# Optimization experiments

Hardware: AMD Instinct MI355X
Metric: run time of the kernel (lower is better)

## Reference

```python
import jax, jax.numpy as jnp
import numpy as np

N, E, IN, H, C, ED = 50000, 800000, 128, 4, 64, 4
NEG_SLOPE = 0.2


def setup_inputs() -> dict:
    key = jax.random.key(0)
    ks = iter(jax.random.split(key, 40))
    def p(shape, s=0.05):
        return jax.random.normal(next(ks), shape, jnp.float32) * s
    inp = dict(
        x=jax.random.normal(next(ks), (N, IN), jnp.float32),
        edge_index=jax.random.randint(next(ks), (2, E), 0, N),
        edge_attr=jax.random.normal(next(ks), (E, ED), jnp.float32),
        # GATConv layer 1 (concat=True)
        W1=p((IN, H * C)), att_src1=p((H, C)), att_dst1=p((H, C)),
        We1=p((ED, H * C)), att_e1=p((H, C)), b1=p((H * C,)),
        g1=jnp.ones((H * C,), jnp.float32), be1=jnp.zeros((H * C,), jnp.float32),
        # GATConv layer 2 (concat=False -> mean over heads)
        W2=p((H * C, H * C)), att_src2=p((H, C)), att_dst2=p((H, C)),
        We2=p((ED, H * C)), att_e2=p((H, C)), b2=p((C,)),
        g2=jnp.ones((C,), jnp.float32), be2=jnp.zeros((C,), jnp.float32),
        # skip / MLP head
        skip_W=p((IN, C)), skip_b=p((C,)),
        fc1_W=p((C, C // 2)), fc1_b=p((C // 2,)),
        fc2_W=p((C // 2, 1)), fc2_b=p((1,)),
    )
    return inp


def _add_self_loops(edge_index, edge_attr, n):
    # PyG GATConv default: add_self_loops=True, fill_value='mean'
    src, dst = edge_index[0], edge_index[1]
    sums = jax.ops.segment_sum(edge_attr, dst, num_segments=n)
    cnt = jax.ops.segment_sum(jnp.ones((edge_attr.shape[0], 1), edge_attr.dtype), dst, num_segments=n)
    mean_attr = sums / jnp.maximum(cnt, 1.0)
    loop = jnp.arange(n)
    src = jnp.concatenate([src, loop])
    dst = jnp.concatenate([dst, loop])
    ea = jnp.concatenate([edge_attr, mean_attr], axis=0)
    return src, dst, ea


def _gat_layer(x, src, dst, ea, W, a_src, a_dst, We, a_e, bias, n, concat):
    xs = (x @ W).reshape(n, H, C)                     # [N,H,C]
    alpha_src = (xs * a_src).sum(-1)                  # [N,H]
    alpha_dst = (xs * a_dst).sum(-1)                  # [N,H]
    ep = (ea @ We).reshape(-1, H, C)                  # [Et,H,C]
    alpha_e = (ep * a_e).sum(-1)                      # [Et,H]
    alpha = jax.nn.leaky_relu(alpha_src[src] + alpha_dst[dst] + alpha_e, NEG_SLOPE)
    # segment softmax over destination nodes
    m = jax.ops.segment_max(alpha, dst, num_segments=n)
    alpha = jnp.exp(alpha - m[dst])
    denom = jax.ops.segment_sum(alpha, dst, num_segments=n)
    alpha = alpha / (denom[dst] + 1e-16)
    out = jax.ops.segment_sum(xs[src] * alpha[:, :, None], dst, num_segments=n)  # [N,H,C]
    out = out.reshape(n, H * C) if concat else out.mean(axis=1)
    return out + bias


def _bn(x, g, b):
    mu = x.mean(0)
    var = x.var(0)
    return (x - mu) * jax.lax.rsqrt(var + 1e-5) * g + b


def reference(x, edge_index, edge_attr, W1, att_src1, att_dst1, We1, att_e1, b1, g1, be1,
              W2, att_src2, att_dst2, We2, att_e2, b2, g2, be2,
              skip_W, skip_b, fc1_W, fc1_b, fc2_W, fc2_b):
    n = x.shape[0]
    src, dst, ea = _add_self_loops(edge_index, edge_attr, n)
    residual = x @ skip_W + skip_b
    h = _gat_layer(x, src, dst, ea, W1, att_src1, att_dst1, We1, att_e1, b1, n, True)
    h = jax.nn.elu(_bn(h, g1, be1))
    h = _gat_layer(h, src, dst, ea, W2, att_src2, att_dst2, We2, att_e2, b2, n, False)
    h = jax.nn.elu(_bn(h, g2, be2))
    h = h + residual
    h = jax.nn.relu(h @ fc1_W + fc1_b)
    h = jax.nn.softplus(h @ fc2_W + fc2_b)
    return h.squeeze(-1)
```

## Files before the change

kernel.cpp:

```cpp
#include <hip/hip_runtime.h>
#include <math.h>

static constexpr int N_NODES = 50000;
static constexpr int N_EDGES = 800000;
static constexpr int IN_F = 128;
static constexpr int CH = 64;
static constexpr int HC = 256;
static constexpr float NEG_SLOPE = 0.2f;

typedef __attribute__((ext_vector_type(8))) short bf16x8;
typedef __attribute__((ext_vector_type(4))) float f32x4;

__device__ __forceinline__ unsigned pack_bf(float a, float b) {
    unsigned ua = __float_as_uint(a) + 0x8000u;
    unsigned ub = __float_as_uint(b) + 0x8000u;
    return __builtin_amdgcn_perm(ub, ua, 0x07060302u);
}
__device__ __forceinline__ float bflo(unsigned u) { return __uint_as_float(u << 16); }
__device__ __forceinline__ float bfhi(unsigned u) { return __uint_as_float(u & 0xffff0000u); }
__device__ __forceinline__ float bfs(unsigned short u) {
    return __uint_as_float((unsigned)u << 16);
}
__device__ __forceinline__ float elu(float v) { return v > 0.f ? v : __expf(v) - 1.0f; }

__device__ __forceinline__ int sigma(int p) { return ((p & 15) << 4) | (p >> 4); }

static constexpr int EB_BLK = (N_EDGES + 255) / 256;
static constexpr int CONV_ITEMS = 106496 + 32;
static constexpr int CONV_BLK = (CONV_ITEMS + 255) / 256;
static constexpr int GEMM_BLKS = (N_NODES + 63) / 64;

__global__ void hist_conv(const int* __restrict__ ei, int* __restrict__ deg,
                          const float* __restrict__ W1, const float* __restrict__ W2,
                          const float* __restrict__ Ws, const float* __restrict__ We1,
                          const float* __restrict__ atte1, const float* __restrict__ We2,
                          const float* __restrict__ atte2, unsigned short* __restrict__ WT1,
                          unsigned short* __restrict__ WT2, unsigned short* __restrict__ WTs,
                          float* __restrict__ weff) {
    if (blockIdx.x < EB_BLK) {
        int e = blockIdx.x * 256 + threadIdx.x;
        if (e < N_EDGES) atomicAdd(&deg[ei[N_EDGES + e]], 1);
        return;
    }
    int t = (blockIdx.x - EB_BLK) * 256 + threadIdx.x;
    if (t < 32768) {
        int k = t >> 8, n = t & 255;
        unsigned u = __float_as_uint(W1[t]) + 0x8000u;
        WT1[n * 128 + k] = (unsigned short)(u >> 16);
    } else if (t < 98304) {
        int u2 = t - 32768;
        int k = u2 >> 8, n = u2 & 255;
        unsigned u = __float_as_uint(W2[u2]) + 0x8000u;
        WT2[n * 256 + sigma(k)] = (unsigned short)(u >> 16);
    } else if (t < 106496) {
        int u2 = t - 98304;
        int k = u2 >> 6, n = u2 & 63;
        unsigned u = __float_as_uint(Ws[u2]) + 0x8000u;
        WTs[n * 128 + k] = (unsigned short)(u >> 16);
    } else if (t < 106496 + 32) {
        int idx = t - 106496;
        const float* We = idx < 16 ? We1 : We2;
        const float* ae = idx < 16 ? atte1 : atte2;
        int j = idx & 15;
        int d = j >> 2, h = j & 3;
        float s = 0.f;
        for (int c = 0; c < CH; ++c) s += We[d * HC + h * CH + c] * ae[h * CH + c];
        weff[idx] = s;
    }
}

__global__ void scan_block(const int* __restrict__ deg, int* __restrict__ rowptr,
                           int* __restrict__ bsum) {
    __shared__ int s[256];
    int tid = threadIdx.x;
    int i = blockIdx.x * 256 + tid;
    int v = (i < N_NODES) ? deg[i] : 0;
    s[tid] = v;
    __syncthreads();
    for (int off = 1; off < 256; off <<= 1) {
        int t = (tid >= off) ? s[tid - off] : 0;
        __syncthreads();
        s[tid] += t;
        __syncthreads();
    }
    if (i < N_NODES) rowptr[i] = s[tid] - v;
    if (tid == 255) bsum[blockIdx.x] = s[255];
}

__global__ void scan_add2(int* __restrict__ rowptr, const int* __restrict__ bsum,
                          int* __restrict__ fillc, int nb) {
    __shared__ int s[256];
    int tid = threadIdx.x;
    int v = (tid < nb) ? bsum[tid] : 0;
    s[tid] = v;
    __syncthreads();
    for (int off = 1; off < 256; off <<= 1) {
        int t = (tid >= off) ? s[tid - off] : 0;
        __syncthreads();
        s[tid] += t;
        __syncthreads();
    }
    int boff = (blockIdx.x == 0) ? 0 : s[blockIdx.x - 1];
    int i = blockIdx.x * 256 + tid;
    if (i < N_NODES) {
        rowptr[i] += boff;
        fillc[i] = 0;
    }
    if (i == N_NODES) rowptr[N_NODES] = N_EDGES;
}

template <int K, bool ABF, bool BN, bool SKIP, bool FILL>
__global__ __launch_bounds__(256) void gemm_mfma_att(
    const void* __restrict__ Av, const unsigned short* __restrict__ BT,
    const float* __restrict__ colsum, const float* __restrict__ g,
    const float* __restrict__ be, float invM,
    const unsigned short* __restrict__ BTs, const float* __restrict__ skip_b,
    float* __restrict__ residual,
    const float* __restrict__ att_src, const float* __restrict__ att_dst,
    unsigned short* __restrict__ xsb, float* __restrict__ asrc, float* __restrict__ adst,
    int M, const int* __restrict__ ei, const float4* __restrict__ ea,
    const int* __restrict__ rowptr, int* __restrict__ fillc, int* __restrict__ csr_src,
    int* __restrict__ csr_dst, float4* __restrict__ eaperm) {
    if constexpr (FILL) {
        if (blockIdx.x >= GEMM_BLKS) {
            int e = (blockIdx.x - GEMM_BLKS) * 256 + threadIdx.x;
            if (e < N_EDGES) {
                int s = ei[e];
                int t = ei[N_EDGES + e];
                int p = atomicAdd(&fillc[t], 1);
                int i = rowptr[t] + p;
                csr_src[i] = s;
                csr_dst[i] = t;
                eaperm[i] = ea[e];
            }
            return;
        }
    }
    constexpr int NT = 16;
    __shared__ float s_scale[256], s_shift[256];
    if constexpr (BN) {
        int c = threadIdx.x;
        int tc = sigma(c);
        float mean = colsum[c] * invM;
        float var = colsum[256 + c] * invM - mean * mean;
        float sc = g[tc] * rsqrtf(var + 1e-5f);
        s_scale[c] = sc;
        s_shift[c] = be[tc] - mean * sc;
        __syncthreads();
    }
    const int lane = threadIdx.x & 63;
    const int wid = threadIdx.x >> 6;
    const int r0 = blockIdx.x * 64 + wid * 16;
    const int lr = lane & 15;
    const int kg = lane >> 4;
    f32x4 acc[NT] = {};
    f32x4 accS[4] = {};
    const float* af = (const float*)Av;
    const unsigned short* ab = (const unsigned short*)Av;
    int rr = r0 + lr;
    if (rr >= M) rr = M - 1;
    const size_t rowoff = (size_t)rr * K + kg * 8;
    const unsigned short* brow = BT + (size_t)lr * K + kg * 8;
    const unsigned short* brow_s = SKIP ? BTs + (size_t)lr * K + kg * 8 : nullptr;
    for (int k0 = 0; k0 < K; k0 += 32) {
        float4 sc0, sc1, sh0, sh1;
        if constexpr (BN) {
            sc0 = *reinterpret_cast<const float4*>(&s_scale[k0 + kg * 8]);
            sc1 = *reinterpret_cast<const float4*>(&s_scale[k0 + kg * 8 + 4]);
            sh0 = *reinterpret_cast<const float4*>(&s_shift[k0 + kg * 8]);
            sh1 = *reinterpret_cast<const float4*>(&s_shift[k0 + kg * 8 + 4]);
        }
        bf16x8 a;
        if constexpr (!ABF) {
            const float4 lo = *reinterpret_cast<const float4*>(af + rowoff + k0);
            const float4 hi = *reinterpret_cast<const float4*>(af + rowoff + k0 + 4);
            union { bf16x8 v; unsigned u[4]; } fa;
            fa.u[0] = pack_bf(lo.x, lo.y);
            fa.u[1] = pack_bf(lo.z, lo.w);
            fa.u[2] = pack_bf(hi.x, hi.y);
            fa.u[3] = pack_bf(hi.z, hi.w);
            a = fa.v;
        } else {
            union { bf16x8 v; unsigned short us[8]; unsigned u[4]; } fa;
            fa.v = *reinterpret_cast<const bf16x8*>(ab + rowoff + k0);
            if constexpr (BN) {
                float f0 = elu(fmaf(bfs(fa.us[0]), sc0.x, sh0.x));
                float f1 = elu(fmaf(bfs(fa.us[1]), sc0.y, sh0.y));
                float f2 = elu(fmaf(bfs(fa.us[2]), sc0.z, sh0.z));
                float f3 = elu(fmaf(bfs(fa.us[3]), sc0.w, sh0.w));
                float f4 = elu(fmaf(bfs(fa.us[4]), sc1.x, sh1.x));
                float f5 = elu(fmaf(bfs(fa.us[5]), sc1.y, sh1.y));
                float f6 = elu(fmaf(bfs(fa.us[6]), sc1.z, sh1.z));
                float f7 = elu(fmaf(bfs(fa.us[7]), sc1.w, sh1.w));
                fa.u[0] = pack_bf(f0, f1);
                fa.u[1] = pack_bf(f2, f3);
                fa.u[2] = pack_bf(f4, f5);
                fa.u[3] = pack_bf(f6, f7);
            }
            a = fa.v;
        }
#pragma unroll
        for (int c = 0; c < NT; ++c) {
            bf16x8 b = *reinterpret_cast<const bf16x8*>(brow + (size_t)c * 16 * K + k0);
            acc[c] = __builtin_amdgcn_mfma_f32_16x16x32_bf16(a, b, acc[c], 0, 0, 0);
        }
        if constexpr (SKIP) {
#pragma unroll
            for (int c = 0; c < 4; ++c) {
                bf16x8 b = *reinterpret_cast<const bf16x8*>(brow_s + (size_t)c * 16 * K + k0);
                accS[c] = __builtin_amdgcn_mfma_f32_16x16x32_bf16(a, b, accS[c], 0, 0, 0);
            }
        }
    }
    float attS[NT], attD[NT];
#pragma unroll
    for (int c = 0; c < NT; ++c) {
        attS[c] = att_src[c * 16 + lr];
        attD[c] = att_dst[c * 16 + lr];
    }
#pragma unroll
    for (int j = 0; j < 4; ++j) {
        int row = r0 + kg * 4 + j;
        bool valid = row < M;
        uint4 ua, ub;
        ua.x = pack_bf(acc[0][j], acc[1][j]);
        ua.y = pack_bf(acc[2][j], acc[3][j]);
        ua.z = pack_bf(acc[4][j], acc[5][j]);
        ua.w = pack_bf(acc[6][j], acc[7][j]);
        ub.x = pack_bf(acc[8][j], acc[9][j]);
        ub.y = pack_bf(acc[10][j], acc[11][j]);
        ub.z = pack_bf(acc[12][j], acc[13][j]);
        ub.w = pack_bf(acc[14][j], acc[15][j]);
        if (valid) {
            uint4* dst = reinterpret_cast<uint4*>(xsb + (size_t)row * HC) + lr * 2;
            dst[0] = ua;
            dst[1] = ub;
        }
        if constexpr (SKIP) {
            if (valid) {
#pragma unroll
                for (int c = 0; c < 4; ++c) {
                    int col = c * 16 + lr;
                    residual[(size_t)row * CH + col] = accS[c][j] + skip_b[col];
                }
            }
        }
#pragma unroll
        for (int h = 0; h < 4; ++h) {
            float ps = acc[4 * h + 0][j] * attS[4 * h + 0] +
                       acc[4 * h + 1][j] * attS[4 * h + 1] +
                       acc[4 * h + 2][j] * attS[4 * h + 2] +
                       acc[4 * h + 3][j] * attS[4 * h + 3];
            float pd = acc[4 * h + 0][j] * attD[4 * h + 0] +
                       acc[4 * h + 1][j] * attD[4 * h + 1] +
                       acc[4 * h + 2][j] * attD[4 * h + 2] +
                       acc[4 * h + 3][j] * attD[4 * h + 3];
#pragma unroll
            for (int mk = 1; mk < 16; mk <<= 1) {
                ps += __shfl_xor(ps, mk);
                pd += __shfl_xor(pd, mk);
            }
            if (valid && lr == 0) {
                asrc[row * 4 + h] = ps;
                adst[row * 4 + h] = pd;
            }
        }
    }
}

__global__ __launch_bounds__(256) void edge_w(
    const int* __restrict__ csr_src, const int* __restrict__ csr_dst,
    const float4* __restrict__ eaperm, const float* __restrict__ weff,
    const float4* __restrict__ asrcv, const float4* __restrict__ adstv,
    uint4* __restrict__ pw) {
    int i = blockIdx.x * 256 + threadIdx.x;
    if (i >= N_EDGES) return;
    int s = csr_src[i];
    int t = csr_dst[i];
    const float4 v = eaperm[i];
    const float4 as4 = asrcv[s];
    const float4 ad4 = adstv[t];
    const float asl[4] = {as4.x, as4.y, as4.z, as4.w};
    const float adl[4] = {ad4.x, ad4.y, ad4.z, ad4.w};
    float p[4], aev[4];
#pragma unroll
    for (int h = 0; h < 4; ++h) {
        float ae = v.x * weff[h] + v.y * weff[4 + h] + v.z * weff[8 + h] + v.w * weff[12 + h];
        float l = asl[h] + adl[h] + ae;
        l = fmaxf(l, NEG_SLOPE * l);
        p[h] = __expf(l);
        aev[h] = ae;
    }
    pw[i] = make_uint4(pack_bf(p[0], p[1]), pack_bf(p[2], p[3]),
                       pack_bf(aev[0], aev[1]), pack_bf(aev[2], aev[3]));
}

template <bool MEAN>
__global__ __launch_bounds__(256) void gat_node(
    const int* __restrict__ rowptr, const int* __restrict__ csr_src,
    const uint4* __restrict__ pw, const float4* __restrict__ asrcv,
    const float4* __restrict__ adstv, const uint2* __restrict__ xsb,
    float* __restrict__ zbuf, void* __restrict__ outp) {
    if (blockIdx.x == 0) {
        zbuf[threadIdx.x] = 0.f;
        zbuf[256 + threadIdx.x] = 0.f;
    }
    int t = blockIdx.x * 4 + (threadIdx.x >> 6);
    if (t >= N_NODES) return;
    const int lane = threadIdx.x & 63;
    const int h = lane & 3;
    const unsigned sh = (h & 1) ? 0u : 16u;
    const bool hiW = (h & 2) != 0;
    const int start = rowptr[t], end = rowptr[t + 1];
    const int deg = end - start;
    const uint2* xl = xsb + lane;
    float acc0 = 0.f, acc1 = 0.f, acc2 = 0.f, acc3 = 0.f;
    float psum = 0.f, aesum = 0.f;
    int i = start;
    for (; i + 8 <= end; i += 8) {
        uint2 f[8];
        float p[8], ae[8];
#pragma unroll
        for (int j = 0; j < 8; ++j) {
            int s = csr_src[i + j];
            f[j] = xl[(size_t)s * 64];
            const uint4 w = pw[i + j];
            unsigned pword = hiW ? w.y : w.x;
            unsigned aeword = hiW ? w.w : w.z;
            p[j] = __uint_as_float((pword << sh) & 0xffff0000u);
            ae[j] = __uint_as_float((aeword << sh) & 0xffff0000u);
        }
#pragma unroll
        for (int j = 0; j < 8; ++j) {
            psum += p[j];
            aesum += ae[j];
            acc0 += bflo(f[j].x) * p[j];
            acc1 += bfhi(f[j].x) * p[j];
            acc2 += bflo(f[j].y) * p[j];
            acc3 += bfhi(f[j].y) * p[j];
        }
    }
    for (; i < end; ++i) {
        int s = csr_src[i];
        uint2 f = xl[(size_t)s * 64];
        const uint4 w = pw[i];
        unsigned pword = hiW ? w.y : w.x;
        unsigned aeword = hiW ? w.w : w.z;
        float p = __uint_as_float((pword << sh) & 0xffff0000u);
        float ae = __uint_as_float((aeword << sh) & 0xffff0000u);
        psum += p;
        aesum += ae;
        acc0 += bflo(f.x) * p;
        acc1 += bfhi(f.x) * p;
        acc2 += bflo(f.y) * p;
        acc3 += bfhi(f.y) * p;
    }
    const float inv_deg = deg > 0 ? 1.0f / (float)deg : 1.0f;
    const float4 as4 = asrcv[t];
    const float4 ad4 = adstv[t];
    float asl = h == 0 ? as4.x : h == 1 ? as4.y : h == 2 ? as4.z : as4.w;
    float adl = h == 0 ? ad4.x : h == 1 ? ad4.y : h == 2 ? ad4.z : ad4.w;
    float l = asl + adl + aesum * inv_deg;
    l = fmaxf(l, NEG_SLOPE * l);
    const float pself = __expf(l);
    uint2 sf = xl[(size_t)t * 64];
    acc0 += bflo(sf.x) * pself;
    acc1 += bfhi(sf.x) * pself;
    acc2 += bflo(sf.y) * pself;
    acc3 += bfhi(sf.y) * pself;
    const float inv = 1.0f / (psum + pself + 1e-16f);
    acc0 *= inv; acc1 *= inv; acc2 *= inv; acc3 *= inv;
    if constexpr (MEAN) {
        acc0 += __shfl_xor(acc0, 1); acc0 += __shfl_xor(acc0, 2);
        acc1 += __shfl_xor(acc1, 1); acc1 += __shfl_xor(acc1, 2);
        acc2 += __shfl_xor(acc2, 1); acc2 += __shfl_xor(acc2, 2);
        acc3 += __shfl_xor(acc3, 1); acc3 += __shfl_xor(acc3, 2);
        if (h == 0) {
            int q = lane >> 2;
            float* o = reinterpret_cast<float*>(outp) + (size_t)t * CH + q;
            o[0] = 0.25f * acc0;
            o[16] = 0.25f * acc1;
            o[32] = 0.25f * acc2;
            o[48] = 0.25f * acc3;
        }
    } else {
        reinterpret_cast<uint2*>(outp)[(size_t)t * 64 + lane] =
            make_uint2(pack_bf(acc0, acc1), pack_bf(acc2, acc3));
    }
}

__global__ void colstats_bf(const unsigned short* __restrict__ X, float* __restrict__ sum,
                            float* __restrict__ sumsq, int M) {
    int c = threadIdx.x;
    int r0 = blockIdx.x * 256;
    int r1 = min(M, r0 + 256);
    float s = 0.f, q = 0.f;
    for (int r = r0; r < r1; ++r) {
        float v = bfs(X[(size_t)r * HC + c]);
        s += v;
        q += v * v;
    }
    atomicAdd(&sum[c], s);
    atomicAdd(&sumsq[c], q);
}

template <int F>
__global__ void colstats(const float* __restrict__ X, float* __restrict__ sum,
                         float* __restrict__ sumsq, int M) {
    const int NG = 256 / F;
    int c = threadIdx.x % F;
    int g = threadIdx.x / F;
    int r0 = blockIdx.x * 256;
    int r1 = min(M, r0 + 256);
    float s = 0.f, q = 0.f;
    for (int r = r0 + g; r < r1; r += NG) {
        float v = X[(size_t)r * F + c];
        s += v;
        q += v * v;
    }
    atomicAdd(&sum[c], s);
    atomicAdd(&sumsq[c], q);
}

__global__ __launch_bounds__(256) void head_mlp(
    const float* __restrict__ h2, const float* __restrict__ colsum,
    const float* __restrict__ g2, const float* __restrict__ be2, float invM,
    const float* __restrict__ residual, const float* __restrict__ fc1W,
    const float* __restrict__ fc1b, const float* __restrict__ fc2W,
    const float* __restrict__ fc2b, float* __restrict__ out) {
    __shared__ float s_sc[CH], s_sh[CH];
    if (threadIdx.x < CH) {
        int c = threadIdx.x;
        float mean = colsum[c] * invM;
        float var = colsum[256 + c] * invM - mean * mean;
        float sc = g2[c] * rsqrtf(var + 1e-5f);
        s_sc[c] = sc;
        s_sh[c] = be2[c] - mean * sc;
    }
    __syncthreads();
    int n = blockIdx.x * 4 + (threadIdx.x >> 6);
    if (n >= N_NODES) return;
    int w = threadIdx.x >> 6;
    int lane = threadIdx.x & 63;
    __shared__ float hrow[4][64];
    float v = fmaf(h2[(size_t)n * CH + lane], s_sc[lane], s_sh[lane]);
    v = elu(v) + residual[(size_t)n * CH + lane];
    hrow[w][lane] = v;
    float p = 0.f;
    if (lane < 32) {
        float acc = fc1b[lane];
#pragma unroll
        for (int k = 0; k < CH; ++k) acc = fmaf(hrow[w][k], fc1W[k * 32 + lane], acc);
        acc = fmaxf(acc, 0.f);
        p = acc * fc2W[lane];
    }
    for (int off = 16; off > 0; off >>= 1) p += __shfl_down(p, off);
    if (lane == 0) {
        float z = p + fc2b[0];
        out[n] = z > 20.f ? z : log1pf(expf(z));
    }
}

extern "C" void kernel_launch(void* const* d_in, const int* in_sizes, int n_in, void* d_out,
                              int out_size, void* d_ws, size_t ws_size, hipStream_t stream) {
    const float* x        = (const float*)d_in[0];
    const int*   ei       = (const int*)d_in[1];
    const float* ea       = (const float*)d_in[2];
    const float* W1       = (const float*)d_in[3];
    const float* att_src1 = (const float*)d_in[4];
    const float* att_dst1 = (const float*)d_in[5];
    const float* We1      = (const float*)d_in[6];
    const float* att_e1   = (const float*)d_in[7];
    const float* g1       = (const float*)d_in[9];
    const float* be1      = (const float*)d_in[10];
    const float* W2       = (const float*)d_in[11];
    const float* att_src2 = (const float*)d_in[12];
    const float* att_dst2 = (const float*)d_in[13];
    const float* We2      = (const float*)d_in[14];
    const float* att_e2   = (const float*)d_in[15];
    const float* g2       = (const float*)d_in[17];
    const float* be2      = (const float*)d_in[18];
    const float* skip_W   = (const float*)d_in[19];
    const float* skip_b   = (const float*)d_in[20];
    const float* fc1_W    = (const float*)d_in[21];
    const float* fc1_b    = (const float*)d_in[22];
    const float* fc2_W    = (const float*)d_in[23];
    const float* fc2_b    = (const float*)d_in[24];
    float* out = (float*)d_out;

    float* wsf = (float*)d_ws;
    size_t off = 0;
    auto take = [&](size_t n) {
        float* p = wsf + off;
        off += n;
        return p;
    };
    unsigned short* xsb  = (unsigned short*)take((size_t)N_NODES * HC / 2);
    unsigned short* aggb = (unsigned short*)take((size_t)N_NODES * HC / 2);
    uint4* pw       = (uint4*)take((size_t)N_EDGES * 4);
    float4* eaperm  = (float4*)take((size_t)N_EDGES * 4);
    int* csr_src    = (int*)take(N_EDGES);
    int* csr_dst    = (int*)take(N_EDGES);
    int* rowptr     = (int*)take(N_NODES + 1);
    int* degfill    = (int*)take(N_NODES);
    int* bsum       = (int*)take(256);
    float* asrc     = take(N_NODES * 4);
    float* adst     = take(N_NODES * 4);
    float* residual = take((size_t)N_NODES * CH);
    float* h2       = take((size_t)N_NODES * CH);
    float* weff     = take(32);
    float* colsum   = take(HC);
    float* colsq    = take(HC);
    unsigned short* WT1 = (unsigned short*)take(IN_F * HC / 2);
    unsigned short* WT2 = (unsigned short*)take(HC * HC / 2);
    unsigned short* WTs = (unsigned short*)take(IN_F * CH / 2);

    const int NBLK = (N_NODES + 255) / 256;
    const int NODE4 = (N_NODES + 3) / 4;
    const float invM = 1.0f / N_NODES;

    hipMemsetAsync(degfill, 0, N_NODES * sizeof(int), stream);
    hist_conv<<<EB_BLK + CONV_BLK, 256, 0, stream>>>(ei, degfill, W1, W2, skip_W, We1,
                                                     att_e1, We2, att_e2, WT1, WT2, WTs, weff);
    scan_block<<<NBLK, 256, 0, stream>>>(degfill, rowptr, bsum);
    scan_add2<<<(N_NODES + 256) / 256, 256, 0, stream>>>(rowptr, bsum, degfill, NBLK);

    gemm_mfma_att<IN_F, false, false, true, true>
        <<<GEMM_BLKS + EB_BLK, 256, 0, stream>>>(
            x, WT1, nullptr, nullptr, nullptr, 0.f, WTs, skip_b, residual, att_src1,
            att_dst1, xsb, asrc, adst, N_NODES, ei, (const float4*)ea, rowptr, degfill,
            csr_src, csr_dst, eaperm);
    edge_w<<<EB_BLK, 256, 0, stream>>>(csr_src, csr_dst, eaperm, weff, (const float4*)asrc,
                                       (const float4*)adst, pw);
    gat_node<false><<<NODE4, 256, 0, stream>>>(rowptr, csr_src, pw, (const float4*)asrc,
                                               (const float4*)adst, (const uint2*)xsb,
                                               colsum, aggb);
    colstats_bf<<<NBLK, 256, 0, stream>>>(aggb, colsum, colsq, N_NODES);

    gemm_mfma_att<HC, true, true, false, false><<<GEMM_BLKS, 256, 0, stream>>>(
        aggb, WT2, colsum, g1, be1, invM, nullptr, nullptr, nullptr, att_src2, att_dst2,
        xsb, asrc, adst, N_NODES, nullptr, nullptr, nullptr, nullptr, nullptr, nullptr,
        nullptr);
    edge_w<<<EB_BLK, 256, 0, stream>>>(csr_src, csr_dst, eaperm, weff + 16,
                                       (const float4*)asrc, (const float4*)adst, pw);
    gat_node<true><<<NODE4, 256, 0, stream>>>(rowptr, csr_src, pw, (const float4*)asrc,
                                              (const float4*)adst, (const uint2*)xsb,
                                              colsum, h2);
    colstats<CH><<<NBLK, 256, 0, stream>>>(h2, colsum, colsq, N_NODES);

    head_mlp<<<NODE4, 256, 0, stream>>>(h2, colsum, g2, be2, invM, residual, fc1_W, fc1_b,
                                        fc2_W, fc2_b, out);
}
```

Measured before the change: 497.1 us.

## Scatter edge weights via position map instead of permuting edge attributes

The CSR fill moves out of the first GEMM into a separate kernel. It now records only csr_src and a per-edge position index, dropping the permuted csr_dst and edge_attr arrays. edge_w reads the original edge arrays in coalesced order and scatters its packed output to the CSR slot. This cuts the 16-byte random writes of edge_attr and the per-edge dst storage, but it adds an extra kernel launch, loses the overlap of the fill with the GEMM, and makes the pw writes scattered.

```diff
diff --git a/kernel.cpp b/kernel.cpp
--- a/kernel.cpp
+++ b/kernel.cpp
@@ -109,7 +109,20 @@
     if (i == N_NODES) rowptr[N_NODES] = N_EDGES;
 }
 
-template <int K, bool ABF, bool BN, bool SKIP, bool FILL>
+__global__ void csr_fill(const int* __restrict__ ei, const int* __restrict__ rowptr,
+                         int* __restrict__ fillc, int* __restrict__ csr_src,
+                         int* __restrict__ pos) {
+    int e = blockIdx.x * blockDim.x + threadIdx.x;
+    if (e >= N_EDGES) return;
+    int s = ei[e];
+    int t = ei[N_EDGES + e];
+    int p = atomicAdd(&fillc[t], 1);
+    int i = rowptr[t] + p;
+    csr_src[i] = s;
+    pos[e] = i;
+}
+
+template <int K, bool ABF, bool BN, bool SKIP>
 __global__ __launch_bounds__(256) void gemm_mfma_att(
     const void* __restrict__ Av, const unsigned short* __restrict__ BT,
     const float* __restrict__ colsum, const float* __restrict__ g,
@@ -118,24 +131,7 @@
     float* __restrict__ residual,
     const float* __restrict__ att_src, const float* __restrict__ att_dst,
     unsigned short* __restrict__ xsb, float* __restrict__ asrc, float* __restrict__ adst,
-    int M, const int* __restrict__ ei, const float4* __restrict__ ea,
-    const int* __restrict__ rowptr, int* __restrict__ fillc, int* __restrict__ csr_src,
-    int* __restrict__ csr_dst, float4* __restrict__ eaperm) {
-    if constexpr (FILL) {
-        if (blockIdx.x >= GEMM_BLKS) {
-            int e = (blockIdx.x - GEMM_BLKS) * 256 + threadIdx.x;
-            if (e < N_EDGES) {
-                int s = ei[e];
-                int t = ei[N_EDGES + e];
-                int p = atomicAdd(&fillc[t], 1);
-                int i = rowptr[t] + p;
-                csr_src[i] = s;
-                csr_dst[i] = t;
-                eaperm[i] = ea[e];
-            }
-            return;
-        }
-    }
+    int M) {
     constexpr int NT = 16;
     __shared__ float s_scale[256], s_shift[256];
     if constexpr (BN) {
@@ -269,15 +265,14 @@
 }
 
 __global__ __launch_bounds__(256) void edge_w(
-    const int* __restrict__ csr_src, const int* __restrict__ csr_dst,
-    const float4* __restrict__ eaperm, const float* __restrict__ weff,
-    const float4* __restrict__ asrcv, const float4* __restrict__ adstv,
-    uint4* __restrict__ pw) {
-    int i = blockIdx.x * 256 + threadIdx.x;
-    if (i >= N_EDGES) return;
-    int s = csr_src[i];
-    int t = csr_dst[i];
-    const float4 v = eaperm[i];
+    const int* __restrict__ ei, const float4* __restrict__ ea, const int* __restrict__ pos,
+    const float* __restrict__ weff, const float4* __restrict__ asrcv,
+    const float4* __restrict__ adstv, uint4* __restrict__ pw) {
+    int e = blockIdx.x * 256 + threadIdx.x;
+    if (e >= N_EDGES) return;
+    int s = ei[e];
+    int t = ei[N_EDGES + e];
+    const float4 v = ea[e];
     const float4 as4 = asrcv[s];
     const float4 ad4 = adstv[t];
     const float asl[4] = {as4.x, as4.y, as4.z, as4.w};
@@ -291,8 +286,8 @@
         p[h] = __expf(l);
         aev[h] = ae;
     }
-    pw[i] = make_uint4(pack_bf(p[0], p[1]), pack_bf(p[2], p[3]),
-                       pack_bf(aev[0], aev[1]), pack_bf(aev[2], aev[3]));
+    pw[pos[e]] = make_uint4(pack_bf(p[0], p[1]), pack_bf(p[2], p[3]),
+                            pack_bf(aev[0], aev[1]), pack_bf(aev[2], aev[3]));
 }
 
 template <bool MEAN>
@@ -498,9 +493,8 @@
     unsigned short* xsb  = (unsigned short*)take((size_t)N_NODES * HC / 2);
     unsigned short* aggb = (unsigned short*)take((size_t)N_NODES * HC / 2);
     uint4* pw       = (uint4*)take((size_t)N_EDGES * 4);
-    float4* eaperm  = (float4*)take((size_t)N_EDGES * 4);
     int* csr_src    = (int*)take(N_EDGES);
-    int* csr_dst    = (int*)take(N_EDGES);
+    int* pos        = (int*)take(N_EDGES);
     int* rowptr     = (int*)take(N_NODES + 1);
     int* degfill    = (int*)take(N_NODES);
     int* bsum       = (int*)take(256);
@@ -524,24 +518,22 @@
                                                      att_e1, We2, att_e2, WT1, WT2, WTs, weff);
     scan_block<<<NBLK, 256, 0, stream>>>(degfill, rowptr, bsum);
     scan_add2<<<(N_NODES + 256) / 256, 256, 0, stream>>>(rowptr, bsum, degfill, NBLK);
-
-    gemm_mfma_att<IN_F, false, false, true, true>
-        <<<GEMM_BLKS + EB_BLK, 256, 0, stream>>>(
-            x, WT1, nullptr, nullptr, nullptr, 0.f, WTs, skip_b, residual, att_src1,
-            att_dst1, xsb, asrc, adst, N_NODES, ei, (const float4*)ea, rowptr, degfill,
-            csr_src, csr_dst, eaperm);
-    edge_w<<<EB_BLK, 256, 0, stream>>>(csr_src, csr_dst, eaperm, weff, (const float4*)asrc,
+    csr_fill<<<EB_BLK, 256, 0, stream>>>(ei, rowptr, degfill, csr_src, pos);
+
+    gemm_mfma_att<IN_F, false, false, true><<<GEMM_BLKS, 256, 0, stream>>>(
+        x, WT1, nullptr, nullptr, nullptr, 0.f, WTs, skip_b, residual, att_src1, att_dst1,
+        xsb, asrc, adst, N_NODES);
+    edge_w<<<EB_BLK, 256, 0, stream>>>(ei, (const float4*)ea, pos, weff, (const float4*)asrc,
                                        (const float4*)adst, pw);
     gat_node<false><<<NODE4, 256, 0, stream>>>(rowptr, csr_src, pw, (const float4*)asrc,
                                                (const float4*)adst, (const uint2*)xsb,
                                                colsum, aggb);
     colstats_bf<<<NBLK, 256, 0, stream>>>(aggb, colsum, colsq, N_NODES);
 
-    gemm_mfma_att<HC, true, true, false, false><<<GEMM_BLKS, 256, 0, stream>>>(
+    gemm_mfma_att<HC, true, true, false><<<GEMM_BLKS, 256, 0, stream>>>(
         aggb, WT2, colsum, g1, be1, invM, nullptr, nullptr, nullptr, att_src2, att_dst2,
-        xsb, asrc, adst, N_NODES, nullptr, nullptr, nullptr, nullptr, nullptr, nullptr,
-        nullptr);
-    edge_w<<<EB_BLK, 256, 0, stream>>>(csr_src, csr_dst, eaperm, weff + 16,
+        xsb, asrc, adst, N_NODES);
+    edge_w<<<EB_BLK, 256, 0, stream>>>(ei, (const float4*)ea, pos, weff + 16,
                                        (const float4*)asrc, (const float4*)adst, pw);
     gat_node<true><<<NODE4, 256, 0, stream>>>(rowptr, csr_src, pw, (const float4*)asrc,
                                               (const float4*)adst, (const uint2*)xsb,
```

New measurement: 544.0 us. 9.4% more time.
